# Kernel tuning notes

Measured on AMD Instinct MI355X. Metric: run time of the kernel, lower is better.

## Reference

```python
import jax, jax.numpy as jnp
import numpy as np

NUM_CLASSES = 19
LOSS_WEIGHT = 0.5
EPS_MEAN = 1e-6   # added to per-class pixel counts
EPS_PD = 1e-6     # torch F.pairwise_distance eps (added to the difference)


def setup_inputs() -> dict:
    key = jax.random.key(0)
    k1, k2, k3 = jax.random.split(key, 3)
    N, C, H, W = 8, 19, 512, 1024
    preds_S = jax.random.normal(k1, (N, C, H, W), dtype=jnp.float32)
    preds_T = jax.random.normal(k2, (N, C, H, W), dtype=jnp.float32)
    gt = jax.random.randint(k3, (N, 1, H, W), 0, NUM_CLASSES, dtype=jnp.int32)
    return {"preds_S": preds_S, "preds_T": preds_T, "gt": gt}


def _class_means(feats, labels, counts_inv):
    # feats: [N, HW, C], labels: [N, HW] int, counts_inv: [N, K]
    seg = jax.vmap(lambda x, s: jax.ops.segment_sum(x, s, num_segments=NUM_CLASSES))
    sums = seg(feats, labels)                      # [N, K, C]
    return sums * counts_inv[..., None]            # [N, K, C]


def reference(preds_S, preds_T, gt):
    N, C, H, W = preds_S.shape
    # gt: F.interpolate(gt.float(), [H,W], bilinear, align_corners=False).int()
    gt_f = jax.image.resize(gt.astype(jnp.float32), (N, 1, H, W), method="bilinear")
    labels = gt_f.astype(jnp.int32).reshape(N, H * W)            # [N, HW]

    # per-class counts (shared between S and T since masks are identical)
    ones = jnp.ones((N, H * W), dtype=jnp.float32)
    seg1 = jax.vmap(lambda x, s: jax.ops.segment_sum(x, s, num_segments=NUM_CLASSES))
    counts = seg1(ones, labels)                                   # [N, K]
    counts_inv = 1.0 / (counts + EPS_MEAN)

    xs = jnp.transpose(preds_S.reshape(N, C, H * W), (0, 2, 1))   # [N, HW, C]
    xt = jnp.transpose(preds_T.reshape(N, C, H * W), (0, 2, 1))
    v_S = _class_means(xs, labels, counts_inv)                    # [N, K, C]
    v_T = _class_means(xt, labels, counts_inv)

    # pairwise euclidean distances between class prototypes (torch eps on diff)
    d_S = v_S[:, :, None, :] - v_S[:, None, :, :] + EPS_PD        # [N, K, K, C]
    d_T = v_T[:, :, None, :] - v_T[:, None, :, :] + EPS_PD
    e_S = jnp.sqrt(jnp.sum(d_S * d_S, axis=-1))                   # [N, K, K]
    e_T = jnp.sqrt(jnp.sum(d_T * d_T, axis=-1))

    tri = jnp.triu(jnp.ones((NUM_CLASSES, NUM_CLASSES), dtype=jnp.float32), k=1)
    per_pair = 0.5 * (e_T - e_S) ** 2                             # [N, K, K]
    loss = jnp.mean(jnp.sum(per_pair * tri, axis=(1, 2)))         # mean over batch
    return LOSS_WEIGHT * loss
```

## Files before the change

kernel.cpp:

```cpp
#include <hip/hip_runtime.h>

#define NCLS 19
#define HWSZ (512*1024)
#define NB   8
#define CHUNK 2048
#define TPX   64
#define NT    (CHUNK/TPX)
#define EPSM  1e-6f
#define EPSPD 1e-6f

#define ROWP 20
#define COLP 32
#define SUMS_ELEMS (NB*2*ROWP*COLP)

#define REGION 160
#define DHALF  640

typedef short bf16x8 __attribute__((ext_vector_type(8)));
typedef float f32x16 __attribute__((ext_vector_type(16)));
typedef unsigned uint4v __attribute__((ext_vector_type(4)));

#define CVT(pA, pB, HI, LO) {                                                      \
    const unsigned uA = __builtin_bit_cast(unsigned, pA);                          \
    const unsigned uB = __builtin_bit_cast(unsigned, pB);                          \
    HI = __builtin_amdgcn_perm(uB, uA, 0x07060302u);                               \
    const float fa = (pA) - __builtin_bit_cast(float, uA & 0xFFFF0000u);           \
    const float fb = (pB) - __builtin_bit_cast(float, uB & 0xFFFF0000u);           \
    LO = __builtin_amdgcn_perm(__builtin_bit_cast(unsigned, fb),                   \
                               __builtin_bit_cast(unsigned, fa), 0x07060302u); }

#define BBIT(word, sh, ei) { const unsigned lb_ = ((word) >> (sh)) & 255u;         \
    B[ei] = (lb_ == ur) ? (short)0x3F80 : (short)0; }

#define SGI(j) { const int f_ = (j)*64 + lane;                                     \
    const int row_ = f_ >> 3, g_ = f_ & 7;                                         \
    const int lb_ = ((g_ >> 2) << 1) | (g_ & 1);                                   \
    const int kg_ = (g_ >> 1) & 1;                                                 \
    lidx##j = lb_*40 + ((kg_*20 + row_) ^ lb_);                                    \
    gp##j = X + ((long)(n*NCLS + (row_ < NCLS ? row_ : 0)))*HWSZ                   \
              + chunk0 + ph*32 + g_*4; }

#define LOADS(set, tt) {                                                           \
    x##set##0 = *(const float4*)(gp0 + (tt)*TPX);                                  \
    x##set##1 = *(const float4*)(gp1 + (tt)*TPX);                                  \
    if (lane < 24) x##set##2 = *(const float4*)(gp2 + (tt)*TPX); }

#define WRITES(set, rg) {                                                          \
    (rg)[lidx0] = x##set##0;                                                       \
    (rg)[lidx1] = x##set##1;                                                       \
    if (lane < 24) (rg)[lidx2] = x##set##2; }

#define KSTEP(cb_, t_, i_, iA, iB) {                                               \
    const uint2 pk = *(const uint2*)(labP + (t_)*TPX + (i_)*16);                   \
    const float4 d0 = (cb_)[iA];                                                   \
    const float4 d1 = (cb_)[iB];                                                   \
    bf16x8 B;                                                                      \
    BBIT(pk.x, 0, 0) BBIT(pk.x, 8, 1) BBIT(pk.x, 16, 2) BBIT(pk.x, 24, 3)         \
    BBIT(pk.y, 0, 4) BBIT(pk.y, 8, 5) BBIT(pk.y, 16, 6) BBIT(pk.y, 24, 7)         \
    unsigned h0, h1, h2, h3, l0_, l1_, l2_, l3_;                                   \
    CVT(d0.x, d0.y, h0, l0_)  CVT(d0.z, d0.w, h1, l1_)                             \
    CVT(d1.x, d1.y, h2, l2_)  CVT(d1.z, d1.w, h3, l3_)                             \
    const bf16x8 hi = __builtin_bit_cast(bf16x8, (uint4v){h0, h1, h2, h3});        \
    const bf16x8 lo = __builtin_bit_cast(bf16x8, (uint4v){l0_, l1_, l2_, l3_});    \
    acc = __builtin_amdgcn_mfma_f32_32x32x16_bf16(hi, B, acc, 0, 0, 0);            \
    acc = __builtin_amdgcn_mfma_f32_32x32x16_bf16(lo, B, acc, 0, 0, 0); }

#define COMPUTE(t_, rg) { KSTEP(rg, t_, 0, idx00, idx01)                           \
                          KSTEP(rg, t_, 1, idx10, idx11) }

#define LDSFENCE { asm volatile("s_waitcnt lgkmcnt(0)" ::: "memory");              \
                   __builtin_amdgcn_sched_barrier(0); }

__global__ __launch_bounds__(256, 4) void icl_sums(
    const float* __restrict__ S, const float* __restrict__ T,
    const int* __restrict__ gt, float* __restrict__ sums)
{
    __shared__ float4 buf4[2*DHALF];
    __shared__ unsigned char labU[CHUNK];
    __shared__ float red[2][ROWP][COLP];

    const int tid = threadIdx.x;
    const int n   = blockIdx.y;
    const long chunk0 = (long)blockIdx.x * CHUNK;

    for (int i = tid; i < 2 * ROWP * COLP; i += 256) ((float*)red)[i] = 0.f;

    {
        const int4* gp = (const int4*)(gt + (long)n * HWSZ + chunk0);
        const int4 a = gp[tid], b = gp[tid + 256];
        ((unsigned*)labU)[tid] = (unsigned)a.x | ((unsigned)a.y << 8) |
                                 ((unsigned)a.z << 16) | ((unsigned)a.w << 24);
        ((unsigned*)labU)[tid + 256] = (unsigned)b.x | ((unsigned)b.y << 8) |
                                       ((unsigned)b.z << 16) | ((unsigned)b.w << 24);
    }
    __syncthreads();

    const int wave = tid >> 6, lane = tid & 63;
    const int r  = lane & 31;
    const int kg = lane >> 5;
    const bool isT = wave >= 2;
    const int  ph  = wave & 1;
    const unsigned ur = (unsigned)r;

    const float* X = isT ? T : S;

    int lidx0, lidx1, lidx2;
    const float *gp0, *gp1, *gp2;
    SGI(0) SGI(1) SGI(2)

    float4* reg0 = buf4 + wave * REGION;
    float4* reg1 = buf4 + DHALF + wave * REGION;

    if (lane < 16) {
        const int d_ = lane >> 3, rem = lane & 7, lb = rem >> 1, kg_ = rem & 1;
        buf4[d_*DHALF + wave*REGION + lb*40 + (((kg_*20) + 19) ^ lb)] =
            make_float4(1.f, 1.f, 1.f, 1.f);
    }

    const int sr = (r < 20) ? r : r - 12;
    const int sl = kg * 20 + sr;
    const int idx00 = 0*40 + (sl ^ 0);
    const int idx01 = 1*40 + (sl ^ 1);
    const int idx10 = 2*40 + (sl ^ 2);
    const int idx11 = 3*40 + (sl ^ 3);

    const unsigned char* labP = labU + ph * 32 + kg * 8;

    f32x16 acc = {0,0,0,0,0,0,0,0,0,0,0,0,0,0,0,0};
    float4 xA0, xA1, xA2, xB0, xB1, xB2;

    LOADS(A, 0)
    LOADS(B, 1)

    for (int t = 0; t < NT; t += 2) {
        WRITES(A, reg0)
        if (t + 2 < NT) { LOADS(A, t + 2) }
        LDSFENCE
        COMPUTE(t, reg0)

        WRITES(B, reg1)
        if (t + 3 < NT) { LOADS(B, t + 3) }
        LDSFENCE
        COMPUTE(t + 1, reg1)
    }

#pragma unroll
    for (int e = 0; e < 16; ++e) {
        const int row = (e & 3) + 8 * (e >> 2) + 4 * kg;
        if (row < ROWP) atomicAdd(&red[isT ? 1 : 0][row][r], acc[e]);
    }
    __syncthreads();

    float* gs = sums + (long)n * 2 * ROWP * COLP;
    for (int i = tid; i < 2 * ROWP * COLP; i += 256) {
        if ((i & 31) < NCLS) atomicAdd(&gs[i], ((const float*)red)[i]);
    }
}

__global__ __launch_bounds__(256) void icl_final(
    const float* __restrict__ sums, float* __restrict__ out)
{
    __shared__ float v[NB][2][NCLS][NCLS];
    __shared__ float red2[256];
    const int tid = threadIdx.x;

    for (int i = tid; i < NB * 2 * NCLS * NCLS; i += 256) {
        const int c = i % NCLS;
        const int k = (i / NCLS) % NCLS;
        const int t = (i / (NCLS * NCLS)) % 2;
        const int n = i / (2 * NCLS * NCLS);
        const float cnt = sums[((n * 2 + 0) * ROWP + NCLS) * COLP + k];
        const float val = sums[((n * 2 + t) * ROWP + c) * COLP + k];
        v[n][t][k][c] = val * (1.f / (cnt + EPSM));
    }
    __syncthreads();

    float acc = 0.f;
    const int NPAIR = NCLS * (NCLS - 1) / 2;
    for (int i = tid; i < NB * NPAIR; i += 256) {
        const int n = i / NPAIR;
        int rem = i % NPAIR;
        int k1 = 0;
        while (rem >= NCLS - 1 - k1) { rem -= NCLS - 1 - k1; ++k1; }
        const int k2 = k1 + 1 + rem;
        float ss = 0.f, st = 0.f;
#pragma unroll
        for (int c = 0; c < NCLS; ++c) {
            const float ds = v[n][0][k1][c] - v[n][0][k2][c] + EPSPD;
            const float dt = v[n][1][k1][c] - v[n][1][k2][c] + EPSPD;
            ss = fmaf(ds, ds, ss);
            st = fmaf(dt, dt, st);
        }
        const float e = sqrtf(st) - sqrtf(ss);
        acc += 0.5f * e * e;
    }

    red2[tid] = acc;
    __syncthreads();
    for (int s = 128; s > 0; s >>= 1) {
        if (tid < s) red2[tid] += red2[tid + s];
        __syncthreads();
    }
    if (tid == 0) out[0] = 0.5f * red2[0] / (float)NB;
}

extern "C" void kernel_launch(void* const* d_in, const int* in_sizes, int n_in,
                              void* d_out, int out_size, void* d_ws, size_t ws_size,
                              hipStream_t stream) {
    const float* S  = (const float*)d_in[0];
    const float* T  = (const float*)d_in[1];
    const int*   gt = (const int*)d_in[2];

    float* sums = (float*)d_ws;
    hipMemsetAsync(d_ws, 0, SUMS_ELEMS * sizeof(float), stream);

    dim3 grid(HWSZ / CHUNK, NB);
    icl_sums<<<grid, 256, 0, stream>>>(S, T, gt, sums);
    icl_final<<<1, 256, 0, stream>>>(sums, (float*)d_out);
}
```

Baseline: 163.2 us.

## Software-pipeline LDS fragment reads ahead of MFMA compute in sums kernel

Restructures the main loop so the LDS reads of label bytes and feature fragments for the next tile are issued into register sets before the current tile's MFMAs run. The explicit lgkmcnt(0) fence and sched barrier are dropped, so the compiler can overlap LDS latency with compute, and a prologue and epilogue handle the loop edges. This costs extra registers for the double fragment sets and leans on the compiler to insert correct waits. Each wave writes and reads its own LDS region, so the missing barrier is meant to stay safe.

After: 534.3 us. +227.4%, slower.

```diff
diff --git a/kernel.cpp b/kernel.cpp
--- a/kernel.cpp
+++ b/kernel.cpp
@@ -50,10 +50,16 @@
     (rg)[lidx1] = x##set##1;                                                       \
     if (lane < 24) (rg)[lidx2] = x##set##2; }
 
-#define KSTEP(cb_, t_, i_, iA, iB) {                                               \
-    const uint2 pk = *(const uint2*)(labP + (t_)*TPX + (i_)*16);                   \
-    const float4 d0 = (cb_)[iA];                                                   \
-    const float4 d1 = (cb_)[iB];                                                   \
+#define FR_DECL(s) float4 fd##s##0, fd##s##1, fd##s##2, fd##s##3;                  \
+                   uint2 fp##s##0, fp##s##1;
+
+#define DSREAD(s, rg, t_) {                                                        \
+    fp##s##0 = *(const uint2*)(labP + (t_)*TPX);                                   \
+    fp##s##1 = *(const uint2*)(labP + (t_)*TPX + 16);                              \
+    fd##s##0 = (rg)[idx00]; fd##s##1 = (rg)[idx01];                                \
+    fd##s##2 = (rg)[idx10]; fd##s##3 = (rg)[idx11]; }
+
+#define KSTEP2(pk, d0, d1) {                                                       \
     bf16x8 B;                                                                      \
     BBIT(pk.x, 0, 0) BBIT(pk.x, 8, 1) BBIT(pk.x, 16, 2) BBIT(pk.x, 24, 3)         \
     BBIT(pk.y, 0, 4) BBIT(pk.y, 8, 5) BBIT(pk.y, 16, 6) BBIT(pk.y, 24, 7)         \
@@ -65,11 +71,8 @@
     acc = __builtin_amdgcn_mfma_f32_32x32x16_bf16(hi, B, acc, 0, 0, 0);            \
     acc = __builtin_amdgcn_mfma_f32_32x32x16_bf16(lo, B, acc, 0, 0, 0); }
 
-#define COMPUTE(t_, rg) { KSTEP(rg, t_, 0, idx00, idx01)                           \
-                          KSTEP(rg, t_, 1, idx10, idx11) }
-
-#define LDSFENCE { asm volatile("s_waitcnt lgkmcnt(0)" ::: "memory");              \
-                   __builtin_amdgcn_sched_barrier(0); }
+#define COMPUTE2(s) { KSTEP2(fp##s##0, fd##s##0, fd##s##1)                         \
+                      KSTEP2(fp##s##1, fd##s##2, fd##s##3) }
 
 __global__ __launch_bounds__(256, 4) void icl_sums(
     const float* __restrict__ S, const float* __restrict__ T,
@@ -128,21 +131,35 @@
 
     f32x16 acc = {0,0,0,0,0,0,0,0,0,0,0,0,0,0,0,0};
     float4 xA0, xA1, xA2, xB0, xB1, xB2;
-
-    LOADS(A, 0)
-    LOADS(B, 1)
-
-    for (int t = 0; t < NT; t += 2) {
+    FR_DECL(C) FR_DECL(N)
+
+    LOADS(A, 0) LOADS(B, 1)
+    WRITES(A, reg0)
+    LOADS(A, 2)
+    DSREAD(C, reg0, 0)
+    WRITES(B, reg1)
+    LOADS(B, 3)
+    DSREAD(N, reg1, 1)
+
+    for (int t = 0; t < NT - 4; t += 2) {
+        COMPUTE2(C)
         WRITES(A, reg0)
-        if (t + 2 < NT) { LOADS(A, t + 2) }
-        LDSFENCE
-        COMPUTE(t, reg0)
-
+        LOADS(A, t + 4)
+        DSREAD(C, reg0, t + 2)
+        COMPUTE2(N)
         WRITES(B, reg1)
-        if (t + 3 < NT) { LOADS(B, t + 3) }
-        LDSFENCE
-        COMPUTE(t + 1, reg1)
-    }
+        LOADS(B, t + 5)
+        DSREAD(N, reg1, t + 3)
+    }
+
+    COMPUTE2(C)
+    WRITES(A, reg0)
+    DSREAD(C, reg0, NT - 2)
+    COMPUTE2(N)
+    WRITES(B, reg1)
+    DSREAD(N, reg1, NT - 1)
+    COMPUTE2(C)
+    COMPUTE2(N)
 
 #pragma unroll
     for (int e = 0; e < 16; ++e) {
```

## Share block-wide LDS staging with 4-deep register prefetch and block barriers

Applied to the files above, without the earlier changes.

Replaces per-wave private LDS regions, where each wave loaded its own S or T slice, with one block-wide staging buffer. All 256 threads cooperatively load both S and T tiles each step, and a block barrier sits before and after compute. Register prefetch depth goes from 2 to 4 sets, and launch bounds drop from 4 to 3 blocks per CU to make room for the extra registers. This aims to keep more global loads in flight, at the cost of two block barriers per step and lower occupancy.

New measurement: 155.5 us. 4.7% less time.

```diff
diff --git a/kernel.cpp b/kernel.cpp
--- a/kernel.cpp
+++ b/kernel.cpp
@@ -12,9 +12,7 @@
 #define ROWP 20
 #define COLP 32
 #define SUMS_ELEMS (NB*2*ROWP*COLP)
-
-#define REGION 160
-#define DHALF  640
+#define F4T  (NCLS*TPX/4)
 
 typedef short bf16x8 __attribute__((ext_vector_type(8)));
 typedef float f32x16 __attribute__((ext_vector_type(16)));
@@ -32,28 +30,32 @@
 #define BBIT(word, sh, ei) { const unsigned lb_ = ((word) >> (sh)) & 255u;         \
     B[ei] = (lb_ == ur) ? (short)0x3F80 : (short)0; }
 
-#define SGI(j) { const int f_ = (j)*64 + lane;                                     \
-    const int row_ = f_ >> 3, g_ = f_ & 7;                                         \
-    const int lb_ = ((g_ >> 2) << 1) | (g_ & 1);                                   \
-    const int kg_ = (g_ >> 1) & 1;                                                 \
-    lidx##j = lb_*40 + ((kg_*20 + row_) ^ lb_);                                    \
-    gp##j = X + ((long)(n*NCLS + (row_ < NCLS ? row_ : 0)))*HWSZ                   \
-              + chunk0 + ph*32 + g_*4; }
+#define SGI(j) { int f = tid + (j)*256;                                            \
+    if (f >= F4T) f = F4T - 1;                                                     \
+    const int row_ = f >> 4, g_ = f & 15;                                          \
+    const int blk_ = ((g_ >> 2) << 1) | (g_ & 1);                                  \
+    const int slot_ = (((g_ >> 1) & 1) * 20) + row_;                               \
+    widx##j = blk_*40 + (slot_ ^ blk_);                                            \
+    const long po_ = ((long)(n*NCLS + row_))*HWSZ + chunk0 + (g_ << 2);            \
+    sp##j = S + po_;  tp##j = T + po_; }
+
+#define SG_DECL(set) float4 s##set##0, s##set##1, t##set##0, t##set##1;
 
 #define LOADS(set, tt) {                                                           \
-    x##set##0 = *(const float4*)(gp0 + (tt)*TPX);                                  \
-    x##set##1 = *(const float4*)(gp1 + (tt)*TPX);                                  \
-    if (lane < 24) x##set##2 = *(const float4*)(gp2 + (tt)*TPX); }
-
-#define WRITES(set, rg) {                                                          \
-    (rg)[lidx0] = x##set##0;                                                       \
-    (rg)[lidx1] = x##set##1;                                                       \
-    if (lane < 24) (rg)[lidx2] = x##set##2; }
-
-#define KSTEP(cb_, t_, i_, iA, iB) {                                               \
-    const uint2 pk = *(const uint2*)(labP + (t_)*TPX + (i_)*16);                   \
-    const float4 d0 = (cb_)[iA];                                                   \
-    const float4 d1 = (cb_)[iB];                                                   \
+    s##set##0 = *(const float4*)(sp0 + (long)(tt)*TPX);                            \
+    t##set##0 = *(const float4*)(tp0 + (long)(tt)*TPX);                            \
+    if (act1) {                                                                    \
+        s##set##1 = *(const float4*)(sp1 + (long)(tt)*TPX);                        \
+        t##set##1 = *(const float4*)(tp1 + (long)(tt)*TPX); } }
+
+#define WRITES(set) {                                                              \
+    buf4[widx0]       = s##set##0;                                                 \
+    buf4[widx0 + 320] = t##set##0;                                                 \
+    if (act1) {                                                                    \
+        buf4[widx1]       = s##set##1;                                             \
+        buf4[widx1 + 320] = t##set##1; } }
+
+#define KSTEP2(pk, d0, d1) {                                                       \
     bf16x8 B;                                                                      \
     BBIT(pk.x, 0, 0) BBIT(pk.x, 8, 1) BBIT(pk.x, 16, 2) BBIT(pk.x, 24, 3)         \
     BBIT(pk.y, 0, 4) BBIT(pk.y, 8, 5) BBIT(pk.y, 16, 6) BBIT(pk.y, 24, 7)         \
@@ -65,17 +67,26 @@
     acc = __builtin_amdgcn_mfma_f32_32x32x16_bf16(hi, B, acc, 0, 0, 0);            \
     acc = __builtin_amdgcn_mfma_f32_32x32x16_bf16(lo, B, acc, 0, 0, 0); }
 
-#define COMPUTE(t_, rg) { KSTEP(rg, t_, 0, idx00, idx01)                           \
-                          KSTEP(rg, t_, 1, idx10, idx11) }
-
-#define LDSFENCE { asm volatile("s_waitcnt lgkmcnt(0)" ::: "memory");              \
-                   __builtin_amdgcn_sched_barrier(0); }
-
-__global__ __launch_bounds__(256, 4) void icl_sums(
+#define COMPUTE(t_) {                                                              \
+    const uint2 pk0 = *(const uint2*)(labB + (t_)*TPX);                            \
+    const uint2 pk1 = *(const uint2*)(labB + (t_)*TPX + 16);                       \
+    const float4 a0 = xb4[i00], a1 = xb4[i01];                                     \
+    const float4 b0 = xb4[i10], b1 = xb4[i11];                                     \
+    KSTEP2(pk0, a0, a1)  KSTEP2(pk1, b0, b1) }
+
+#define PHASE(set, t_) {                                                           \
+    WRITES(set)                                                                    \
+    if ((t_) + 4 < NT) { LOADS(set, (t_) + 4) }                                    \
+    asm volatile("s_waitcnt lgkmcnt(0)" ::: "memory");                             \
+    __builtin_amdgcn_s_barrier();                                                  \
+    COMPUTE(t_)                                                                    \
+    __builtin_amdgcn_s_barrier(); }
+
+__global__ __launch_bounds__(256, 3) void icl_sums(
     const float* __restrict__ S, const float* __restrict__ T,
     const int* __restrict__ gt, float* __restrict__ sums)
 {
-    __shared__ float4 buf4[2*DHALF];
+    __shared__ float4 buf4[2*320];
     __shared__ unsigned char labU[CHUNK];
     __shared__ float red[2][ROWP][COLP];
 
@@ -93,7 +104,11 @@
         ((unsigned*)labU)[tid + 256] = (unsigned)b.x | ((unsigned)b.y << 8) |
                                        ((unsigned)b.z << 16) | ((unsigned)b.w << 24);
     }
-    __syncthreads();
+
+    if (tid < 32) {
+        const int blk = tid >> 2, kg_ = (tid >> 1) & 1, tb = tid & 1;
+        buf4[tb*320 + blk*40 + (((kg_*20) + 19) ^ blk)] = make_float4(1.f,1.f,1.f,1.f);
+    }
 
     const int wave = tid >> 6, lane = tid & 63;
     const int r  = lane & 31;
@@ -101,47 +116,34 @@
     const bool isT = wave >= 2;
     const int  ph  = wave & 1;
     const unsigned ur = (unsigned)r;
-
-    const float* X = isT ? T : S;
-
-    int lidx0, lidx1, lidx2;
-    const float *gp0, *gp1, *gp2;
-    SGI(0) SGI(1) SGI(2)
-
-    float4* reg0 = buf4 + wave * REGION;
-    float4* reg1 = buf4 + DHALF + wave * REGION;
-
-    if (lane < 16) {
-        const int d_ = lane >> 3, rem = lane & 7, lb = rem >> 1, kg_ = rem & 1;
-        buf4[d_*DHALF + wave*REGION + lb*40 + (((kg_*20) + 19) ^ lb)] =
-            make_float4(1.f, 1.f, 1.f, 1.f);
-    }
+    const bool act1 = (tid + 256) < F4T;
+
+    int widx0, widx1;
+    const float *sp0, *tp0, *sp1, *tp1;
+    SGI(0) SGI(1)
+    SG_DECL(A) SG_DECL(B) SG_DECL(C) SG_DECL(D)
 
     const int sr = (r < 20) ? r : r - 12;
     const int sl = kg * 20 + sr;
-    const int idx00 = 0*40 + (sl ^ 0);
-    const int idx01 = 1*40 + (sl ^ 1);
-    const int idx10 = 2*40 + (sl ^ 2);
-    const int idx11 = 3*40 + (sl ^ 3);
-
-    const unsigned char* labP = labU + ph * 32 + kg * 8;
+    const int i00 = (ph*4+0)*40 + (sl ^ (ph*4+0));
+    const int i01 = (ph*4+1)*40 + (sl ^ (ph*4+1));
+    const int i10 = (ph*4+2)*40 + (sl ^ (ph*4+2));
+    const int i11 = (ph*4+3)*40 + (sl ^ (ph*4+3));
+
+    const float4* xb4 = buf4 + (isT ? 320 : 0);
+    const unsigned char* labB = labU + ph * 32 + kg * 8;
 
     f32x16 acc = {0,0,0,0,0,0,0,0,0,0,0,0,0,0,0,0};
-    float4 xA0, xA1, xA2, xB0, xB1, xB2;
-
-    LOADS(A, 0)
-    LOADS(B, 1)
-
-    for (int t = 0; t < NT; t += 2) {
-        WRITES(A, reg0)
-        if (t + 2 < NT) { LOADS(A, t + 2) }
-        LDSFENCE
-        COMPUTE(t, reg0)
-
-        WRITES(B, reg1)
-        if (t + 3 < NT) { LOADS(B, t + 3) }
-        LDSFENCE
-        COMPUTE(t + 1, reg1)
+
+    __syncthreads();
+
+    LOADS(A, 0) LOADS(B, 1) LOADS(C, 2) LOADS(D, 3)
+
+    for (int t = 0; t < NT; t += 4) {
+        PHASE(A, t)
+        PHASE(B, t + 1)
+        PHASE(C, t + 2)
+        PHASE(D, t + 3)
     }
 
 #pragma unroll
```
